# Performance work log

Hardware: AMD Instinct MI355X
Metric: run time of the kernel (lower is better)

The kernel has to match this reference:

```python
import jax, jax.numpy as jnp
import numpy as np

B, S, D, E, TOP_K = 4, 4096, 2048, 64, 2

def setup_inputs() -> dict:
    key = jax.random.key(0)
    k1, k2, k3, k4 = jax.random.split(key, 4)
    return {
        "mh_output": jax.random.normal(k1, (B, S, D), dtype=jnp.float32),
        "W_route": jax.random.normal(k2, (D, E), dtype=jnp.float32) * (1.0 / np.sqrt(D)),
        "b_route": jnp.zeros((E,), dtype=jnp.float32),
        "W_noise": jax.random.normal(k3, (D, E), dtype=jnp.float32) * (1.0 / np.sqrt(D)),
        "b_noise": jnp.zeros((E,), dtype=jnp.float32),
        "noise": jax.random.normal(k4, (B, S, E), dtype=jnp.float32),
    }

def reference(mh_output, W_route, b_route, W_noise, b_noise, noise):
    # logits / noise logits: [B, S, E]
    logits = jnp.einsum("bsd,de->bse", mh_output, W_route) + b_route
    noise_logits = jnp.einsum("bsd,de->bse", mh_output, W_noise) + b_noise
    noisy_logits = logits + noise * jax.nn.softplus(noise_logits)

    top_vals, indices = jax.lax.top_k(noisy_logits, TOP_K)  # [B,S,K]

    # scatter top-k values into a -inf-filled tensor, then softmax
    flat_vals = top_vals.reshape(-1, TOP_K)
    flat_idx = indices.reshape(-1, TOP_K)
    n_tok = flat_idx.shape[0]
    rows = jnp.arange(n_tok)[:, None]
    sparse = jnp.full((n_tok, E), -jnp.inf, dtype=noisy_logits.dtype)
    sparse = sparse.at[rows, flat_idx].set(flat_vals)
    probs = jax.nn.softmax(sparse, axis=-1).reshape(noisy_logits.shape)
    return probs, indices
```

## Files before the change

kernel.cpp:

```cpp
#include <hip/hip_runtime.h>
#include <math.h>

#define M_TOK 16384
#define D_DIM 2048
#define E_EXP 64
#define BM    32
#define NT_H  16
#define FRAG_B 1040
#define TILE_B (12 * FRAG_B)
#define SMEM_BYTES (4 * TILE_B)
#define LL_LD 132

typedef float         f32x16 __attribute__((ext_vector_type(16)));
typedef short         bf16x8 __attribute__((ext_vector_type(8)));
typedef unsigned int  uint;

#define MFMA32(a, b, c) __builtin_amdgcn_mfma_f32_32x32x16_bf16((a), (b), (c), 0, 0, 0)

__device__ __forceinline__ unsigned short bfrne(float f) {
    unsigned int u = __float_as_uint(f);
    return (unsigned short)((u + 0x7fffu + ((u >> 16) & 1u)) >> 16);
}
__device__ __forceinline__ float bfhi(unsigned short h) {
    return __uint_as_float((unsigned int)h << 16);
}

__device__ __forceinline__ bool beats(float va, int ia, float vb, int ib) {
    return (va > vb) || (va == vb && ia < ib);
}

__global__ __launch_bounds__(256) void prep_w(
    const float* __restrict__ Wr, const float* __restrict__ Wn,
    unsigned short* __restrict__ Wg)
{
    const int g     = blockIdx.x * 256 + threadIdx.x;
    const int lane  = g & 63;
    const int ch    = (g >> 6) & 3;
    const int kstep = g >> 8;
    const int col   = ch * 32 + (lane & 31);
    const float* __restrict__ W = (col < 64) ? Wr : Wn;
    const int colL  = col & 63;
    const int kbase = kstep * 16 + (lane >> 5) * 8;

    bf16x8 o0, o1, o2;
    #pragma unroll
    for (int j = 0; j < 8; ++j) {
        const float w = W[(size_t)(kbase + j) * E_EXP + colL];
        const unsigned short h0 = bfrne(w);
        const float r  = w - bfhi(h0);
        const unsigned short h1 = bfrne(r);
        const float r2 = r - bfhi(h1);
        const unsigned short h2 = bfrne(r2);
        o0[j] = (short)h0; o1[j] = (short)h1; o2[j] = (short)h2;
    }
    #pragma unroll
    for (int p = 0; p < 3; ++p) {
        const size_t idx = (((size_t)kstep * 3 + p) * 4 + ch) * 64 + lane;
        const bf16x8 o = (p == 0) ? o0 : (p == 1) ? o1 : o2;
        *(bf16x8*)(Wg + idx * 8) = o;
    }
}

__device__ __forceinline__ void load_b_half(const unsigned short* __restrict__ Wg,
                                            int t, int s0, int wc, int lane,
                                            bf16x8 (&Bv)[2][3])
{
    #pragma unroll
    for (int s = 0; s < 2; ++s) {
        const int kstep = t * 4 + s0 + s;
        #pragma unroll
        for (int p = 0; p < 3; ++p) {
            const size_t idx = (((size_t)kstep * 3 + p) * 4 + wc);
            Bv[s][p] = *(const bf16x8*)(Wg + (idx << 9) + lane * 8);
        }
    }
}

__device__ __forceinline__ void load_a(const float* __restrict__ A, int tokBase,
                                       int t, int tid, float4& x)
{
    const int row = tid >> 4;
    const int kc  = tid & 15;
    x = *(const float4*)(A + (size_t)(tokBase + row) * D_DIM + t * 64 + kc * 4);
}

__device__ __forceinline__ void cvt_store(char* tbase, int tid, const float4& x)
{
    const float v[4] = {x.x, x.y, x.z, x.w};
    uint t0[4], t1[4]; unsigned short h2[4];
    #pragma unroll
    for (int j = 0; j < 4; ++j) {
        const uint u = __float_as_uint(v[j]);
        t0[j] = u & 0xffff0000u;
        const float r = v[j] - __uint_as_float(t0[j]);
        const uint ru = __float_as_uint(r);
        t1[j] = ru & 0xffff0000u;
        const float r2 = r - __uint_as_float(t1[j]);
        h2[j] = bfrne(r2);
    }
    uint2 w0, w1, w2;
    w0.x = (t0[0] >> 16) | t0[1];  w0.y = (t0[2] >> 16) | t0[3];
    w1.x = (t1[0] >> 16) | t1[1];  w1.y = (t1[2] >> 16) | t1[3];
    w2.x = (uint)h2[0] | ((uint)h2[1] << 16);
    w2.y = (uint)h2[2] | ((uint)h2[3] << 16);

    const int row   = tid >> 4;
    const int kc    = tid & 15;
    const int kstep = kc >> 2;
    const int hoct  = (kc >> 1) & 1;
    const int half  = kc & 1;
    const int l     = hoct * 32 + row;
    char* p = tbase + kstep * (3 * FRAG_B) + l * 16 + half * 8;
    *(uint2*)(p)              = w0;
    *(uint2*)(p + FRAG_B)     = w1;
    *(uint2*)(p + 2 * FRAG_B) = w2;
}

__device__ __forceinline__ void compute_half(const char* tbase, int s0, int lane,
                                             const bf16x8 (&Bv)[2][3],
                                             f32x16& acch, f32x16& accl)
{
    const char* ap = tbase + lane * 16;
    #pragma unroll
    for (int s = 0; s < 2; ++s) {
        const int f = (s0 + s) * 3;
        const bf16x8 a0 = *(const bf16x8*)(ap + (f + 0) * FRAG_B);
        const bf16x8 a1 = *(const bf16x8*)(ap + (f + 1) * FRAG_B);
        const bf16x8 a2 = *(const bf16x8*)(ap + (f + 2) * FRAG_B);
        acch = MFMA32(a0, Bv[s][0], acch);
        accl = MFMA32(a0, Bv[s][1], accl);
        accl = MFMA32(a1, Bv[s][0], accl);
        accl = MFMA32(a1, Bv[s][1], accl);
        accl = MFMA32(a0, Bv[s][2], accl);
        accl = MFMA32(a2, Bv[s][0], accl);
    }
}

__global__ __launch_bounds__(512) void fused_router(
    const float* __restrict__ A,
    const unsigned short* __restrict__ Wg,
    const float* __restrict__ br, const float* __restrict__ bn,
    const float* __restrict__ noise,
    float* __restrict__ probs, float* __restrict__ idxo)
{
    __shared__ __align__(16) char smem[SMEM_BYTES];

    const int tid  = threadIdx.x;
    const int lane = tid & 63;
    const int wid  = tid >> 6;
    const int wc   = wid & 3;
    const int kh   = wid >> 2;
    const int tokBase = blockIdx.x * BM;

    f32x16 acch, accl;
    #pragma unroll
    for (int r = 0; r < 16; ++r) { acch[r] = 0.f; accl[r] = 0.f; }

    char* st0a = smem;
    char* st0b = smem + TILE_B;
    char* st1a = smem + 2 * TILE_B;
    char* st1b = smem + 3 * TILE_B;
    const char* myBuf0 = smem + (kh * 2 + 0) * TILE_B;
    const char* myBuf1 = smem + (kh * 2 + 1) * TILE_B;

    float4 x0, x1, y0, y1;
    bf16x8 Bv[2][3];

    load_a(A, tokBase, 0,        tid, x0);
    load_a(A, tokBase, NT_H,     tid, x1);
    cvt_store(st0a, tid, x0);
    cvt_store(st1a, tid, x1);
    load_a(A, tokBase, 1,        tid, x0);
    load_a(A, tokBase, NT_H + 1, tid, x1);
    __syncthreads();

    #pragma unroll 1
    for (int it2 = 0; it2 < NT_H / 2; ++it2) {
        const int itA = 2 * it2;
        const int tA  = kh * NT_H + itA;

        load_b_half(Wg, tA, 0, wc, lane, Bv);
        cvt_store(st0b, tid, x0);
        cvt_store(st1b, tid, x1);
        if (itA + 2 < NT_H) {
            load_a(A, tokBase, itA + 2,        tid, y0);
            load_a(A, tokBase, NT_H + itA + 2, tid, y1);
        }
        compute_half(myBuf0, 0, lane, Bv, acch, accl);
        load_b_half(Wg, tA, 2, wc, lane, Bv);
        compute_half(myBuf0, 2, lane, Bv, acch, accl);
        __syncthreads();

        load_b_half(Wg, tA + 1, 0, wc, lane, Bv);
        if (itA + 2 < NT_H) { cvt_store(st0a, tid, y0); cvt_store(st1a, tid, y1); }
        if (itA + 3 < NT_H) {
            load_a(A, tokBase, itA + 3,        tid, x0);
            load_a(A, tokBase, NT_H + itA + 3, tid, x1);
        }
        compute_half(myBuf1, 0, lane, Bv, acch, accl);
        load_b_half(Wg, tA + 1, 2, wc, lane, Bv);
        compute_half(myBuf1, 2, lane, Bv, acch, accl);
        __syncthreads();
    }

    float (*Ll)[BM][LL_LD] = (float (*)[BM][LL_LD])smem;
    {
        const int col   = wc * 32 + (lane & 31);
        const int rbase = 4 * (lane >> 5);
        #pragma unroll
        for (int r = 0; r < 16; ++r) {
            const int row = (r & 3) + 8 * (r >> 2) + rbase;
            Ll[kh][row][col] = acch[r] + accl[r];
        }
    }
    __syncthreads();

    const int token = tid >> 4;
    const int s16   = tid & 15;
    const int tokG  = tokBase + token;

    float v0 = -INFINITY, v1 = -INFINITY;
    int i0 = 0, i1 = 0;
    {
        const float4 n4 = *(const float4*)(noise + (size_t)tokG * E_EXP + s16 * 4);
        const float4 b4 = *(const float4*)(br + s16 * 4);
        const float4 c4 = *(const float4*)(bn + s16 * 4);
        const float4 la = *(const float4*)(&Ll[0][token][s16 * 4]);
        const float4 lb = *(const float4*)(&Ll[1][token][s16 * 4]);
        const float4 ma = *(const float4*)(&Ll[0][token][64 + s16 * 4]);
        const float4 mb = *(const float4*)(&Ll[1][token][64 + s16 * 4]);
        const float nv[4] = {n4.x, n4.y, n4.z, n4.w};
        const float bv[4] = {b4.x, b4.y, b4.z, b4.w};
        const float cv[4] = {c4.x, c4.y, c4.z, c4.w};
        const float lv[4] = {la.x + lb.x, la.y + lb.y, la.z + lb.z, la.w + lb.w};
        const float mv[4] = {ma.x + mb.x, ma.y + mb.y, ma.z + mb.z, ma.w + mb.w};
        #pragma unroll
        for (int j = 0; j < 4; ++j) {
            const int e = s16 * 4 + j;
            const float lg = lv[j] + bv[j];
            const float nl = mv[j] + cv[j];
            const float sp = fmaxf(nl, 0.0f) + log1pf(expf(-fabsf(nl)));
            const float v  = fmaf(nv[j], sp, lg);
            if (beats(v, e, v0, i0))      { v1 = v0; i1 = i0; v0 = v; i0 = e; }
            else if (beats(v, e, v1, i1)) { v1 = v;  i1 = e; }
        }
    }
    #pragma unroll
    for (int m = 1; m < 16; m <<= 1) {
        const float w0 = __shfl_xor(v0, m), w1 = __shfl_xor(v1, m);
        const int   j0 = __shfl_xor(i0, m), j1 = __shfl_xor(i1, m);
        if (beats(v0, i0, w0, j0)) {
            if (!beats(v1, i1, w0, j0)) { v1 = w0; i1 = j0; }
        } else {
            if (beats(v0, i0, w1, j1)) { v1 = v0; i1 = i0; }
            else                       { v1 = w1; i1 = j1; }
            v0 = w0; i0 = j0;
        }
    }
    const float e1  = expf(v1 - v0);
    const float den = 1.0f + e1;
    const float p0 = 1.0f / den;
    const float p1 = e1 / den;

    float out[4];
    #pragma unroll
    for (int j = 0; j < 4; ++j) {
        const int e = s16 * 4 + j;
        out[j] = (e == i0) ? p0 : ((e == i1) ? p1 : 0.0f);
    }
    *(float4*)(probs + (size_t)tokG * E_EXP + s16 * 4) =
        make_float4(out[0], out[1], out[2], out[3]);
    if (s16 == 0)
        *(float2*)(idxo + (size_t)tokG * 2) = make_float2((float)i0, (float)i1);
}

extern "C" void kernel_launch(void* const* d_in, const int* in_sizes, int n_in,
                              void* d_out, int out_size, void* d_ws, size_t ws_size,
                              hipStream_t stream) {
    (void)in_sizes; (void)n_in; (void)out_size; (void)ws_size;
    const float* A  = (const float*)d_in[0];
    const float* Wr = (const float*)d_in[1];
    const float* br = (const float*)d_in[2];
    const float* Wn = (const float*)d_in[3];
    const float* bn = (const float*)d_in[4];
    const float* nz = (const float*)d_in[5];

    float* probs = (float*)d_out;
    float* idxo  = probs + (size_t)M_TOK * E_EXP;

    unsigned short* Wg = (unsigned short*)d_ws;

    prep_w<<<128, 256, 0, stream>>>(Wr, Wn, Wg);
    fused_router<<<M_TOK / BM, 512, 0, stream>>>(A, Wg, br, bn, nz, probs, idxo);
}
```

Measured before the change: 230.3 us.

## Double-buffer B fragments in registers and use lightweight LDS barriers with setprio

The main loop now keeps two register sets of weight fragments (Bx/By), so the next B half-tile is prefetched from global memory while the current one feeds the MFMAs, instead of loading then immediately consuming. __syncthreads is replaced with a barrier that waits only on LDS counters, which lets outstanding global loads stay in flight across the barrier. MFMA sections are wrapped in s_setprio to favour the compute phases, and launch bounds now request 4 blocks per CU. The extra fragment registers raise register pressure, and the occupancy hint may force spills.

```diff
diff --git a/kernel.cpp b/kernel.cpp
--- a/kernel.cpp
+++ b/kernel.cpp
@@ -8,8 +8,8 @@
 #define NT_H  16
 #define FRAG_B 1040
 #define TILE_B (12 * FRAG_B)
+#define LL_LD 132
 #define SMEM_BYTES (4 * TILE_B)
-#define LL_LD 132
 
 typedef float         f32x16 __attribute__((ext_vector_type(16)));
 typedef short         bf16x8 __attribute__((ext_vector_type(8)));
@@ -27,6 +27,12 @@
 
 __device__ __forceinline__ bool beats(float va, int ia, float vb, int ib) {
     return (va > vb) || (va == vb && ia < ib);
+}
+
+__device__ __forceinline__ void block_sync_lds() {
+    asm volatile("s_waitcnt lgkmcnt(0)" ::: "memory");
+    __builtin_amdgcn_s_barrier();
+    asm volatile("" ::: "memory");
 }
 
 __global__ __launch_bounds__(256) void prep_w(
@@ -116,11 +122,11 @@
     *(uint2*)(p + 2 * FRAG_B) = w2;
 }
 
-__device__ __forceinline__ void compute_half(const char* tbase, int s0, int lane,
+__device__ __forceinline__ void compute_half(const char* buf, int s0, int lane,
                                              const bf16x8 (&Bv)[2][3],
                                              f32x16& acch, f32x16& accl)
 {
-    const char* ap = tbase + lane * 16;
+    const char* ap = buf + lane * 16;
     #pragma unroll
     for (int s = 0; s < 2; ++s) {
         const int f = (s0 + s) * 3;
@@ -136,7 +142,7 @@
     }
 }
 
-__global__ __launch_bounds__(512) void fused_router(
+__global__ __launch_bounds__(512, 4) void fused_router(
     const float* __restrict__ A,
     const unsigned short* __restrict__ Wg,
     const float* __restrict__ br, const float* __restrict__ bn,
@@ -156,51 +162,62 @@
     #pragma unroll
     for (int r = 0; r < 16; ++r) { acch[r] = 0.f; accl[r] = 0.f; }
 
-    char* st0a = smem;
-    char* st0b = smem + TILE_B;
-    char* st1a = smem + 2 * TILE_B;
-    char* st1b = smem + 3 * TILE_B;
-    const char* myBuf0 = smem + (kh * 2 + 0) * TILE_B;
-    const char* myBuf1 = smem + (kh * 2 + 1) * TILE_B;
-
-    float4 x0, x1, y0, y1;
-    bf16x8 Bv[2][3];
+    char* s0a = smem;
+    char* s0b = smem + TILE_B;
+    char* s1a = smem + 2 * TILE_B;
+    char* s1b = smem + 3 * TILE_B;
+    const char* myB0 = smem + (kh * 2 + 0) * TILE_B;
+    const char* myB1 = smem + (kh * 2 + 1) * TILE_B;
+
+    bf16x8 Bx[2][3], By[2][3];
+    float4 x0, x1;
 
     load_a(A, tokBase, 0,        tid, x0);
     load_a(A, tokBase, NT_H,     tid, x1);
-    cvt_store(st0a, tid, x0);
-    cvt_store(st1a, tid, x1);
+    cvt_store(s0a, tid, x0);
+    cvt_store(s1a, tid, x1);
     load_a(A, tokBase, 1,        tid, x0);
     load_a(A, tokBase, NT_H + 1, tid, x1);
-    __syncthreads();
+    load_b_half(Wg, kh * NT_H, 0, wc, lane, Bx);
+    block_sync_lds();
 
     #pragma unroll 1
-    for (int it2 = 0; it2 < NT_H / 2; ++it2) {
-        const int itA = 2 * it2;
-        const int tA  = kh * NT_H + itA;
-
-        load_b_half(Wg, tA, 0, wc, lane, Bv);
-        cvt_store(st0b, tid, x0);
-        cvt_store(st1b, tid, x1);
-        if (itA + 2 < NT_H) {
-            load_a(A, tokBase, itA + 2,        tid, y0);
-            load_a(A, tokBase, NT_H + itA + 2, tid, y1);
-        }
-        compute_half(myBuf0, 0, lane, Bv, acch, accl);
-        load_b_half(Wg, tA, 2, wc, lane, Bv);
-        compute_half(myBuf0, 2, lane, Bv, acch, accl);
-        __syncthreads();
-
-        load_b_half(Wg, tA + 1, 0, wc, lane, Bv);
-        if (itA + 2 < NT_H) { cvt_store(st0a, tid, y0); cvt_store(st1a, tid, y1); }
-        if (itA + 3 < NT_H) {
-            load_a(A, tokBase, itA + 3,        tid, x0);
-            load_a(A, tokBase, NT_H + itA + 3, tid, x1);
-        }
-        compute_half(myBuf1, 0, lane, Bv, acch, accl);
-        load_b_half(Wg, tA + 1, 2, wc, lane, Bv);
-        compute_half(myBuf1, 2, lane, Bv, acch, accl);
-        __syncthreads();
+    for (int it = 0; it < NT_H; it += 2) {
+        const int tA = kh * NT_H + it;
+
+        cvt_store(s0b, tid, x0);
+        cvt_store(s1b, tid, x1);
+        if (it + 2 < NT_H) {
+            load_a(A, tokBase, it + 2,        tid, x0);
+            load_a(A, tokBase, NT_H + it + 2, tid, x1);
+        }
+        load_b_half(Wg, tA, 2, wc, lane, By);
+        __builtin_amdgcn_s_setprio(1);
+        compute_half(myB0, 0, lane, Bx, acch, accl);
+        __builtin_amdgcn_s_setprio(0);
+        load_b_half(Wg, tA + 1, 0, wc, lane, Bx);
+        __builtin_amdgcn_s_setprio(1);
+        compute_half(myB0, 2, lane, By, acch, accl);
+        __builtin_amdgcn_s_setprio(0);
+        block_sync_lds();
+
+        if (it + 2 < NT_H) {
+            cvt_store(s0a, tid, x0);
+            cvt_store(s1a, tid, x1);
+        }
+        if (it + 3 < NT_H) {
+            load_a(A, tokBase, it + 3,        tid, x0);
+            load_a(A, tokBase, NT_H + it + 3, tid, x1);
+        }
+        load_b_half(Wg, tA + 1, 2, wc, lane, By);
+        __builtin_amdgcn_s_setprio(1);
+        compute_half(myB1, 0, lane, Bx, acch, accl);
+        __builtin_amdgcn_s_setprio(0);
+        if (it + 2 < NT_H) load_b_half(Wg, tA + 2, 0, wc, lane, Bx);
+        __builtin_amdgcn_s_setprio(1);
+        compute_half(myB1, 2, lane, By, acch, accl);
+        __builtin_amdgcn_s_setprio(0);
+        block_sync_lds();
     }
 
     float (*Ll)[BM][LL_LD] = (float (*)[BM][LL_LD])smem;
@@ -213,7 +230,7 @@
             Ll[kh][row][col] = acch[r] + accl[r];
         }
     }
-    __syncthreads();
+    block_sync_lds();
 
     const int token = tid >> 4;
     const int s16   = tid & 15;
```

After: 237.2 us. 3.0% more time.
